# Optimization experiments

Measured on AMD Instinct MI355X. Metric: run time of the kernel, lower is better.

The kernel has to match this reference:

```python
import jax, jax.numpy as jnp
import numpy as np

B, J, H, W, P = 48, 17, 128, 128, 30  # batch, joints, heatmap HxW, max people
N = J * H * W  # flattened tag-map length per image


def setup_inputs() -> dict:
    key = jax.random.key(0)
    k1, k2, k3, k4 = jax.random.split(key, 4)
    outputs = jax.random.normal(k1, (B, 2 * J, H, W), dtype=jnp.float32)
    heatmaps = jax.random.uniform(k2, (B, J, H, W), dtype=jnp.float32)
    idx = jax.random.randint(k3, (B, P, J), 0, N)
    vis = jax.random.randint(k4, (B, P, J), 0, 2)
    joints = jnp.stack([idx, vis], axis=-1).astype(jnp.int64)  # [B,P,J,2]
    return {"outputs": outputs, "heatmaps": heatmaps, "joints": joints}


def _heatmap_mse(pred, gt):
    # mask over (batch, channel): channels whose gt sums to > 0
    mask = (gt.sum(axis=(2, 3)) > 0).astype(pred.dtype)  # [B,C]
    per = ((pred - gt) ** 2).mean(axis=(2, 3))            # [B,C]
    return (per * mask).sum() / mask.sum()


def _ae_loss(tags, joints):
    # tags: [B,N] flattened tag maps; joints: [B,P,J,2] int (idx, visibility)
    idx = joints[..., 0]
    vis = (joints[..., 1] > 0).astype(tags.dtype)         # [B,P,J]
    t = jax.vmap(lambda tg, ix: tg[ix])(tags, idx)        # [B,P,J] gathered tags
    cnt = vis.sum(-1)                                     # [B,P] visible joints per person
    person_valid = cnt > 0
    safe_cnt = jnp.where(person_valid, cnt, 1.0)
    m = (t * vis).sum(-1) / safe_cnt                      # [B,P] per-person mean tag
    per_pull = (vis * (t - m[..., None]) ** 2).sum(-1) / safe_cnt
    per_pull = jnp.where(person_valid, per_pull, 0.0)
    num_tags = person_valid.sum(-1).astype(tags.dtype)    # [B]
    pull = per_pull.sum(-1) / jnp.maximum(num_tags, 1.0)
    # push: all-pairs exp(-(m_i - m_j)^2) over valid persons, minus diagonal (num_tags)
    diff = m[:, :, None] - m[:, None, :]                  # [B,P,P]
    pair_mask = person_valid[:, :, None] & person_valid[:, None, :]
    push_raw = jnp.where(pair_mask, jnp.exp(-diff ** 2), 0.0).sum(axis=(1, 2)) - num_tags
    denom = (num_tags - 1.0) * num_tags
    push = jnp.where(num_tags >= 2.0,
                     push_raw / jnp.where(denom > 0, denom, 1.0) * 0.5,
                     0.0)
    return push, pull


def reference(outputs, heatmaps, joints):
    hm_pred = outputs[:, :J]                   # [B,J,H,W]
    tags = outputs[:, J:].reshape(B, -1)       # [B,N] (tag channels flattened)
    hm_loss = _heatmap_mse(hm_pred, heatmaps)  # scalar (factor 1.0)
    push, pull = _ae_loss(tags, joints)        # [B], [B] (factors 1.0)
    return hm_loss, push, pull
```

## Files before the change

kernel.cpp:

```cpp
#include <hip/hip_runtime.h>
#include <hip/hip_bf16.h>

constexpr int B = 48, J = 17, H = 128, W = 128, P = 30;
constexpr int HW = H * W;
constexpr int NPLANES = B * J;
constexpr int SUBS = 4;
constexpr int CHUNK_FLOATS = HW / SUBS;
constexpr int NCHUNK = NPLANES * SUBS;
constexpr int AE_BLOCKS = B;

__global__ __launch_bounds__(256) void fused_kernel(
        const float* __restrict__ outputs,
        const float* __restrict__ heatmaps,
        const unsigned* __restrict__ joints_u32,
        float2* __restrict__ ws2,
        float* __restrict__ out) {
    int t = threadIdx.x;

    if (blockIdx.x >= AE_BLOCKS) {
        int chunk = blockIdx.x - AE_BLOCKS;
        int plane = chunk >> 2, sub = chunk & 3;
        int b = plane / J, j = plane % J;
        const float4* pred = reinterpret_cast<const float4*>(
            outputs + ((size_t)b * 2 * J + j) * HW + sub * CHUNK_FLOATS);
        const float4* gt = reinterpret_cast<const float4*>(
            heatmaps + (size_t)plane * HW + sub * CHUNK_FLOATS);

        float sq = 0.f, gs = 0.f;
#pragma unroll
        for (int k = 0; k < CHUNK_FLOATS / 4 / 256; ++k) {
            float4 p = pred[t + k * 256];
            float4 g = gt[t + k * 256];
            float d0 = p.x - g.x, d1 = p.y - g.y, d2 = p.z - g.z, d3 = p.w - g.w;
            sq += d0 * d0 + d1 * d1 + d2 * d2 + d3 * d3;
            gs += g.x + g.y + g.z + g.w;
        }
        for (int off = 32; off > 0; off >>= 1) {
            sq += __shfl_xor(sq, off);
            gs += __shfl_xor(gs, off);
        }
        __shared__ float s_sq[4], s_gs[4];
        int wave = t >> 6;
        if ((t & 63) == 0) { s_sq[wave] = sq; s_gs[wave] = gs; }
        __syncthreads();
        if (t == 0) {
            ws2[chunk] = make_float2(s_sq[0] + s_sq[1] + s_sq[2] + s_sq[3],
                                     s_gs[0] + s_gs[1] + s_gs[2] + s_gs[3]);
        }
        return;
    }

    int b = blockIdx.x;
    const float* tags = outputs + ((size_t)b * 2 * J + J) * HW;

    const unsigned* jw = joints_u32 + (size_t)b * P * J * 2 * 2;
    unsigned ob = 0;
#pragma unroll
    for (int k = 0; k < 4; ++k) {
        int i = t + k * 256;
        if (i < P * J * 2) ob |= jw[2 * i + 1];
    }
    __shared__ unsigned s_ob[4];
    for (int off = 32; off > 0; off >>= 1) ob |= (unsigned)__shfl_xor((int)ob, off);
    int wv = t >> 6;
    if ((t & 63) == 0) s_ob[wv] = ob;
    __shared__ float m_sh[P];
    __shared__ int v_sh[P];
    __syncthreads();
    bool is64 = (s_ob[0] | s_ob[1] | s_ob[2] | s_ob[3]) == 0u;

    if (t >= 64) return;
    int lane = t;

    float per_pull = 0.f, m = 0.f;
    int validp = 0;

    if (lane < P) {
        float tv[J];
        int   vv[J];
        int cnt = 0;
        float sum = 0.f;
        if (is64) {
            const long long* jp = reinterpret_cast<const long long*>(joints_u32)
                                  + ((size_t)b * P + lane) * J * 2;
#pragma unroll
            for (int j = 0; j < J; ++j) {
                int idx = (int)jp[2 * j];
                int vis = jp[2 * j + 1] > 0;
                float tval = tags[idx];
                tv[j] = tval; vv[j] = vis;
                cnt += vis;
                sum += vis ? tval : 0.f;
            }
        } else {
            const int* jp = reinterpret_cast<const int*>(joints_u32)
                            + ((size_t)b * P + lane) * J * 2;
#pragma unroll
            for (int j = 0; j < J; ++j) {
                int idx = jp[2 * j];
                int vis = jp[2 * j + 1] > 0;
                float tval = tags[idx];
                tv[j] = tval; vv[j] = vis;
                cnt += vis;
                sum += vis ? tval : 0.f;
            }
        }
        float safe = cnt > 0 ? (float)cnt : 1.f;
        m = sum / safe;
        float pp = 0.f;
#pragma unroll
        for (int j = 0; j < J; ++j) {
            float d = tv[j] - m;
            pp += vv[j] ? d * d : 0.f;
        }
        validp = (cnt > 0) ? 1 : 0;
        per_pull = validp ? pp / safe : 0.f;
        m_sh[lane] = m;
        v_sh[lane] = validp;
    }
    __builtin_amdgcn_s_waitcnt(0);

    float push_p = 0.f;
    if (lane < P && validp) {
#pragma unroll
        for (int k = 0; k < P; ++k) {
            if (v_sh[k]) {
                float d = m - m_sh[k];
                push_p += __expf(-d * d);
            }
        }
    }

    float v0 = per_pull, v1 = push_p, v2 = (float)validp;
    for (int off = 32; off > 0; off >>= 1) {
        v0 += __shfl_xor(v0, off);
        v1 += __shfl_xor(v1, off);
        v2 += __shfl_xor(v2, off);
    }
    if (lane == 0) {
        float num_tags = v2;
        float pull = v0 / fmaxf(num_tags, 1.f);
        float push_raw = v1 - num_tags;
        float denom = (num_tags - 1.f) * num_tags;
        float push = (num_tags >= 2.f) ? (push_raw / (denom > 0.f ? denom : 1.f)) * 0.5f : 0.f;
        out[1 + b] = push;
        out[1 + B + b] = pull;
    }
}

__global__ __launch_bounds__(256) void finalize_kernel(const float2* __restrict__ ws2,
                                                       float* __restrict__ out) {
    int t = threadIdx.x;
    float s = 0.f, c = 0.f;
    for (int p = t; p < NPLANES; p += 256) {
        float sq = 0.f, gs = 0.f;
#pragma unroll
        for (int sub = 0; sub < SUBS; ++sub) {
            float2 v = ws2[p * SUBS + sub];
            sq += v.x; gs += v.y;
        }
        bool mask = gs > 0.f;
        s += mask ? sq * (1.f / HW) : 0.f;
        c += mask ? 1.f : 0.f;
    }
    for (int off = 32; off > 0; off >>= 1) {
        s += __shfl_xor(s, off);
        c += __shfl_xor(c, off);
    }
    __shared__ float s_s[4], s_c[4];
    int wave = t >> 6;
    if ((t & 63) == 0) { s_s[wave] = s; s_c[wave] = c; }
    __syncthreads();
    if (t == 0) {
        out[0] = (s_s[0] + s_s[1] + s_s[2] + s_s[3]) /
                 (s_c[0] + s_c[1] + s_c[2] + s_c[3]);
    }
}

extern "C" void kernel_launch(void* const* d_in, const int* in_sizes, int n_in,
                              void* d_out, int out_size, void* d_ws, size_t ws_size,
                              hipStream_t stream) {
    const float* outputs  = (const float*)d_in[0];
    const float* heatmaps = (const float*)d_in[1];
    const unsigned* joints = (const unsigned*)d_in[2];
    float* out = (float*)d_out;
    float2* ws2 = (float2*)d_ws;

    fused_kernel<<<AE_BLOCKS + NCHUNK, 256, 0, stream>>>(outputs, heatmaps, joints, ws2, out);
    finalize_kernel<<<1, 256, 0, stream>>>(ws2, out);
}
```

Baseline: 24.16 us.

## Fold finalize into main kernel via atomic ticket spin-wait in block zero

Removes the separate finalize kernel launch. Block 0 spin-waits on an atomic ticket counter that each MSE chunk block increments after storing its partial sums, then performs the final reduction. This saves a kernel launch and the gap between kernels, but adds a hipMemsetAsync to reset the ticket and a spinning block that occupies a CU. It also relies on all other blocks being scheduled while block 0 waits.

```diff
diff --git a/kernel.cpp b/kernel.cpp
--- a/kernel.cpp
+++ b/kernel.cpp
@@ -9,16 +9,56 @@
 constexpr int NCHUNK = NPLANES * SUBS;
 constexpr int AE_BLOCKS = B;
 
+union PackF2 { unsigned long long u; float2 f; };
+
 __global__ __launch_bounds__(256) void fused_kernel(
         const float* __restrict__ outputs,
         const float* __restrict__ heatmaps,
         const unsigned* __restrict__ joints_u32,
-        float2* __restrict__ ws2,
+        unsigned* __restrict__ ticket,
+        unsigned long long* __restrict__ parts,
         float* __restrict__ out) {
     int t = threadIdx.x;
 
-    if (blockIdx.x >= AE_BLOCKS) {
-        int chunk = blockIdx.x - AE_BLOCKS;
+    if (blockIdx.x == 0) {
+        if (t == 0) {
+            while (__hip_atomic_load(ticket, __ATOMIC_RELAXED,
+                                     __HIP_MEMORY_SCOPE_AGENT) != (unsigned)NCHUNK) {
+                __builtin_amdgcn_s_sleep(8);
+            }
+            (void)__hip_atomic_load(ticket, __ATOMIC_ACQUIRE, __HIP_MEMORY_SCOPE_AGENT);
+        }
+        __syncthreads();
+
+        float s = 0.f, c = 0.f;
+        for (int p = t; p < NPLANES; p += 256) {
+            float sq = 0.f, gs = 0.f;
+#pragma unroll
+            for (int sub = 0; sub < SUBS; ++sub) {
+                PackF2 pk;
+                pk.u = __hip_atomic_load(parts + p * SUBS + sub, __ATOMIC_RELAXED,
+                                         __HIP_MEMORY_SCOPE_AGENT);
+                sq += pk.f.x; gs += pk.f.y;
+            }
+            if (gs > 0.f) { s += sq * (1.f / HW); c += 1.f; }
+        }
+        for (int off = 32; off > 0; off >>= 1) {
+            s += __shfl_xor(s, off);
+            c += __shfl_xor(c, off);
+        }
+        __shared__ float s_s[4], s_c[4];
+        int wave = t >> 6;
+        if ((t & 63) == 0) { s_s[wave] = s; s_c[wave] = c; }
+        __syncthreads();
+        if (t == 0) {
+            out[0] = (s_s[0] + s_s[1] + s_s[2] + s_s[3]) /
+                     (s_c[0] + s_c[1] + s_c[2] + s_c[3]);
+        }
+        return;
+    }
+
+    if (blockIdx.x > AE_BLOCKS) {
+        int chunk = blockIdx.x - 1 - AE_BLOCKS;
         int plane = chunk >> 2, sub = chunk & 3;
         int b = plane / J, j = plane % J;
         const float4* pred = reinterpret_cast<const float4*>(
@@ -44,13 +84,19 @@
         if ((t & 63) == 0) { s_sq[wave] = sq; s_gs[wave] = gs; }
         __syncthreads();
         if (t == 0) {
-            ws2[chunk] = make_float2(s_sq[0] + s_sq[1] + s_sq[2] + s_sq[3],
-                                     s_gs[0] + s_gs[1] + s_gs[2] + s_gs[3]);
+            PackF2 pk;
+            pk.f = make_float2(s_sq[0] + s_sq[1] + s_sq[2] + s_sq[3],
+                               s_gs[0] + s_gs[1] + s_gs[2] + s_gs[3]);
+            __hip_atomic_store(parts + chunk, pk.u, __ATOMIC_RELAXED,
+                               __HIP_MEMORY_SCOPE_AGENT);
+            asm volatile("s_waitcnt vmcnt(0)" ::: "memory");
+            __hip_atomic_fetch_add(ticket, 1u, __ATOMIC_RELAXED,
+                                   __HIP_MEMORY_SCOPE_AGENT);
         }
         return;
     }
 
-    int b = blockIdx.x;
+    int b = blockIdx.x - 1;
     const float* tags = outputs + ((size_t)b * 2 * J + J) * HW;
 
     const unsigned* jw = joints_u32 + (size_t)b * P * J * 2 * 2;
@@ -148,35 +194,6 @@
     }
 }
 
-__global__ __launch_bounds__(256) void finalize_kernel(const float2* __restrict__ ws2,
-                                                       float* __restrict__ out) {
-    int t = threadIdx.x;
-    float s = 0.f, c = 0.f;
-    for (int p = t; p < NPLANES; p += 256) {
-        float sq = 0.f, gs = 0.f;
-#pragma unroll
-        for (int sub = 0; sub < SUBS; ++sub) {
-            float2 v = ws2[p * SUBS + sub];
-            sq += v.x; gs += v.y;
-        }
-        bool mask = gs > 0.f;
-        s += mask ? sq * (1.f / HW) : 0.f;
-        c += mask ? 1.f : 0.f;
-    }
-    for (int off = 32; off > 0; off >>= 1) {
-        s += __shfl_xor(s, off);
-        c += __shfl_xor(c, off);
-    }
-    __shared__ float s_s[4], s_c[4];
-    int wave = t >> 6;
-    if ((t & 63) == 0) { s_s[wave] = s; s_c[wave] = c; }
-    __syncthreads();
-    if (t == 0) {
-        out[0] = (s_s[0] + s_s[1] + s_s[2] + s_s[3]) /
-                 (s_c[0] + s_c[1] + s_c[2] + s_c[3]);
-    }
-}
-
 extern "C" void kernel_launch(void* const* d_in, const int* in_sizes, int n_in,
                               void* d_out, int out_size, void* d_ws, size_t ws_size,
                               hipStream_t stream) {
@@ -184,8 +201,11 @@
     const float* heatmaps = (const float*)d_in[1];
     const unsigned* joints = (const unsigned*)d_in[2];
     float* out = (float*)d_out;
-    float2* ws2 = (float2*)d_ws;
-
-    fused_kernel<<<AE_BLOCKS + NCHUNK, 256, 0, stream>>>(outputs, heatmaps, joints, ws2, out);
-    finalize_kernel<<<1, 256, 0, stream>>>(ws2, out);
+    unsigned* ticket = (unsigned*)d_ws;
+    unsigned long long* parts =
+        reinterpret_cast<unsigned long long*>((char*)d_ws + 16);
+
+    hipMemsetAsync(d_ws, 0, 4, stream);
+    fused_kernel<<<1 + AE_BLOCKS + NCHUNK, 256, 0, stream>>>(
+        outputs, heatmaps, joints, ticket, parts, out);
 }
```

New measurement: 58.07 us. 2.4x slower.

## Split MSE streaming from AE loss and merge finalize into tail kernel

Applied to the files above, without the earlier changes.

The MSE partial-sum blocks now run alone in their own kernel and use nontemporal vector loads. The associative-embedding loss blocks move into a second kernel, which also holds the final MSE reduction in one extra block. The AE gather work is now serialized after the streaming pass instead of overlapping with it, while the separate finalize kernel goes away. Nontemporal loads are meant to keep the single-use streaming data from polluting the cache.

```diff
diff --git a/kernel.cpp b/kernel.cpp
--- a/kernel.cpp
+++ b/kernel.cpp
@@ -9,43 +9,73 @@
 constexpr int NCHUNK = NPLANES * SUBS;
 constexpr int AE_BLOCKS = B;
 
-__global__ __launch_bounds__(256) void fused_kernel(
+typedef float f32x4 __attribute__((ext_vector_type(4)));
+
+__global__ __launch_bounds__(256) void mse_kernel(
         const float* __restrict__ outputs,
         const float* __restrict__ heatmaps,
+        float2* __restrict__ parts) {
+    int t = threadIdx.x;
+    int chunk = blockIdx.x;
+    int plane = chunk >> 2, sub = chunk & 3;
+    int b = plane / J, j = plane % J;
+    const f32x4* pred = reinterpret_cast<const f32x4*>(
+        outputs + ((size_t)b * 2 * J + j) * HW + sub * CHUNK_FLOATS);
+    const f32x4* gt = reinterpret_cast<const f32x4*>(
+        heatmaps + (size_t)plane * HW + sub * CHUNK_FLOATS);
+
+    float sq = 0.f, gs = 0.f;
+#pragma unroll
+    for (int k = 0; k < CHUNK_FLOATS / 4 / 256; ++k) {
+        f32x4 p = __builtin_nontemporal_load(&pred[t + k * 256]);
+        f32x4 g = __builtin_nontemporal_load(&gt[t + k * 256]);
+        float d0 = p.x - g.x, d1 = p.y - g.y, d2 = p.z - g.z, d3 = p.w - g.w;
+        sq += d0 * d0 + d1 * d1 + d2 * d2 + d3 * d3;
+        gs += g.x + g.y + g.z + g.w;
+    }
+    for (int off = 32; off > 0; off >>= 1) {
+        sq += __shfl_xor(sq, off);
+        gs += __shfl_xor(gs, off);
+    }
+    __shared__ float s_sq[4], s_gs[4];
+    int wave = t >> 6;
+    if ((t & 63) == 0) { s_sq[wave] = sq; s_gs[wave] = gs; }
+    __syncthreads();
+    if (t == 0) {
+        parts[chunk] = make_float2(s_sq[0] + s_sq[1] + s_sq[2] + s_sq[3],
+                                   s_gs[0] + s_gs[1] + s_gs[2] + s_gs[3]);
+    }
+}
+
+__global__ __launch_bounds__(256) void tail_kernel(
+        const float* __restrict__ outputs,
         const unsigned* __restrict__ joints_u32,
-        float2* __restrict__ ws2,
+        const float2* __restrict__ parts,
         float* __restrict__ out) {
     int t = threadIdx.x;
 
-    if (blockIdx.x >= AE_BLOCKS) {
-        int chunk = blockIdx.x - AE_BLOCKS;
-        int plane = chunk >> 2, sub = chunk & 3;
-        int b = plane / J, j = plane % J;
-        const float4* pred = reinterpret_cast<const float4*>(
-            outputs + ((size_t)b * 2 * J + j) * HW + sub * CHUNK_FLOATS);
-        const float4* gt = reinterpret_cast<const float4*>(
-            heatmaps + (size_t)plane * HW + sub * CHUNK_FLOATS);
-
-        float sq = 0.f, gs = 0.f;
+    if (blockIdx.x == AE_BLOCKS) {
+        float s = 0.f, c = 0.f;
+        for (int p = t; p < NPLANES; p += 256) {
+            float sq = 0.f, gs = 0.f;
 #pragma unroll
-        for (int k = 0; k < CHUNK_FLOATS / 4 / 256; ++k) {
-            float4 p = pred[t + k * 256];
-            float4 g = gt[t + k * 256];
-            float d0 = p.x - g.x, d1 = p.y - g.y, d2 = p.z - g.z, d3 = p.w - g.w;
-            sq += d0 * d0 + d1 * d1 + d2 * d2 + d3 * d3;
-            gs += g.x + g.y + g.z + g.w;
+            for (int sub = 0; sub < SUBS; ++sub) {
+                float2 v = parts[p * SUBS + sub];
+                sq += v.x; gs += v.y;
+            }
+            if (gs > 0.f) { s += sq * (1.f / HW); c += 1.f; }
         }
         for (int off = 32; off > 0; off >>= 1) {
-            sq += __shfl_xor(sq, off);
-            gs += __shfl_xor(gs, off);
+            s += __shfl_xor(s, off);
+            c += __shfl_xor(c, off);
         }
-        __shared__ float s_sq[4], s_gs[4];
+        __shared__ float s_s[4], s_c[4];
         int wave = t >> 6;
-        if ((t & 63) == 0) { s_sq[wave] = sq; s_gs[wave] = gs; }
+        if ((t & 63) == 0) { s_s[wave] = s; s_c[wave] = c; }
         __syncthreads();
         if (t == 0) {
-            ws2[chunk] = make_float2(s_sq[0] + s_sq[1] + s_sq[2] + s_sq[3],
-                                     s_gs[0] + s_gs[1] + s_gs[2] + s_gs[3]);
+            out[0] = (s_s[0] + s_s[1] + s_s[2] + s_s[3]) /
+                     (s_c[0] + s_c[1] + s_c[2] + s_c[3]);
         }
         return;
     }
@@ -148,35 +178,6 @@
     }
 }
 
-__global__ __launch_bounds__(256) void finalize_kernel(const float2* __restrict__ ws2,
-                                                       float* __restrict__ out) {
-    int t = threadIdx.x;
-    float s = 0.f, c = 0.f;
-    for (int p = t; p < NPLANES; p += 256) {
-        float sq = 0.f, gs = 0.f;
-#pragma unroll
-        for (int sub = 0; sub < SUBS; ++sub) {
-            float2 v = ws2[p * SUBS + sub];
-            sq += v.x; gs += v.y;
-        }
-        bool mask = gs > 0.f;
-        s += mask ? sq * (1.f / HW) : 0.f;
-        c += mask ? 1.f : 0.f;
-    }
-    for (int off = 32; off > 0; off >>= 1) {
-        s += __shfl_xor(s, off);
-        c += __shfl_xor(c, off);
-    }
-    __shared__ float s_s[4], s_c[4];
-    int wave = t >> 6;
-    if ((t & 63) == 0) { s_s[wave] = s; s_c[wave] = c; }
-    __syncthreads();
-    if (t == 0) {
-        out[0] = (s_s[0] + s_s[1] + s_s[2] + s_s[3]) /
-                 (s_c[0] + s_c[1] + s_c[2] + s_c[3]);
-    }
-}
-
 extern "C" void kernel_launch(void* const* d_in, const int* in_sizes, int n_in,
                               void* d_out, int out_size, void* d_ws, size_t ws_size,
                               hipStream_t stream) {
@@ -184,8 +185,8 @@
     const float* heatmaps = (const float*)d_in[1];
     const unsigned* joints = (const unsigned*)d_in[2];
     float* out = (float*)d_out;
-    float2* ws2 = (float2*)d_ws;
+    float2* parts = (float2*)d_ws;
 
-    fused_kernel<<<AE_BLOCKS + NCHUNK, 256, 0, stream>>>(outputs, heatmaps, joints, ws2, out);
-    finalize_kernel<<<1, 256, 0, stream>>>(ws2, out);
+    mse_kernel<<<NCHUNK, 256, 0, stream>>>(outputs, heatmaps, parts);
+    tail_kernel<<<AE_BLOCKS + 1, 256, 0, stream>>>(outputs, joints, parts, out);
 }
```

Result: slower. 25.11 us (+3.9%).
